# Performance work log

Measured on AMD Instinct MI355X. Metric: run time of the kernel, lower is better.

## Reference

```python
import jax, jax.numpy as jnp
import numpy as np

IN_CH, OUT_CH, K, UP = 512, 256, 3, 2
WSCALE = float(1.0 / np.sqrt(K * K * IN_CH))  # use_wscale gain / sqrt(fan_in), lr_mul=1
ACT_GAIN = float(np.sqrt(2.0))                # lrelu def_gain
CLAMP = 256.0                                  # conv_clamp * runtime_gain(=1)
FIR_PAD = 1                                    # px0+pxt = px1+pxt = 1 (derived in forward)

def _fir_filter():
    # upfirdn2d.setup_filter([1,3,3,1]): outer product then normalize to sum 1
    f1 = jnp.array([1.0, 3.0, 3.0, 1.0], jnp.float32)
    f2 = jnp.outer(f1, f1)
    return f2 / jnp.sum(f2)  # (4,4), sums to 1

def setup_inputs() -> dict:
    key = jax.random.key(0)
    k1, k2 = jax.random.split(key)
    return {
        "x": jax.random.normal(k1, (16, IN_CH, 64, 64), jnp.float32),
        "weight": jax.random.normal(k2, (OUT_CH, IN_CH, K, K), jnp.float32),
        "bias": jnp.zeros((OUT_CH,), jnp.float32),
    }

def _forward(x, weight, bias):
    w = weight * WSCALE  # runtime weight scaling
    # torch conv_transpose2d(x, w.transpose(0,1), stride=UP, padding=0)
    # == lhs-dilated correlation with spatially flipped kernel, pad K-1 each side
    k = w[:, :, ::-1, ::-1]
    y = jax.lax.conv_general_dilated(
        x, k, window_strides=(1, 1),
        padding=((K - 1, K - 1), (K - 1, K - 1)),
        lhs_dilation=(UP, UP),
        dimension_numbers=('NCHW', 'OIHW', 'NCHW'))  # (N, OUT_CH, 129, 129)
    # upfirdn2d(up=1, padding=(1,1,1,1), gain=UP**2):
    # pad, then depthwise conv with flipped filter scaled by gain**(ndim/2)=UP*UP
    f = _fir_filter() * (UP * UP)
    y = jnp.pad(y, ((0, 0), (0, 0), (FIR_PAD, FIR_PAD), (FIR_PAD, FIR_PAD)))
    fk = jnp.broadcast_to(f[::-1, ::-1][None, None], (OUT_CH, 1, 4, 4))
    y = jax.lax.conv_general_dilated(
        y, fk, (1, 1), 'VALID',
        feature_group_count=OUT_CH,
        dimension_numbers=('NCHW', 'OIHW', 'NCHW'))  # (N, OUT_CH, 128, 128)
    # bias_act: bias add, leaky_relu(0.2), gain sqrt(2), clamp +-256
    y = y + bias[None, :, None, None]
    y = jnp.where(y >= 0, y, 0.2 * y) * ACT_GAIN
    return jnp.clip(y, -CLAMP, CLAMP)

def reference(x, weight, bias):
    return _forward(x, weight, bias)
```

## Files before the change

### kernel.cpp

```cpp
#include <hip/hip_runtime.h>
#include <hip/hip_bf16.h>

#define NIMG 16
#define IN_CH 512
#define OUT_CH 256
#define HIN 64
#define HOUT 128
#define HP 66

#define WSCALE 0.014731391f
#define ACT_GAIN 1.41421356237f
#define CLAMP_V 256.0f

typedef __attribute__((ext_vector_type(8))) short bf16x8;
typedef __attribute__((ext_vector_type(4))) float f32x4;
typedef __attribute__((ext_vector_type(16))) float f32x16;

__device__ __constant__ float c_G[2][3][3] = {
    {{0.00f, 0.25f, 0.75f}, {0.75f, 0.75f, 0.25f}, {0.25f, 0.00f, 0.00f}},
    {{0.00f, 0.00f, 0.25f}, {0.25f, 0.75f, 0.75f}, {0.75f, 0.25f, 0.00f}}
};

#define XBF_BYTES ((size_t)NIMG * 64 * HP * HP * 16)
#define EBF_BYTES ((size_t)9 * 64 * 1024 * 16)
#define WS_NEED (XBF_BYTES + EBF_BYTES)

__global__ __launch_bounds__(256) void xpose_kernel(const float* __restrict__ x,
                                                    __hip_bfloat16* __restrict__ xbf) {
    const int n = blockIdx.z;
    const int hp = blockIdx.y;
    const int c0 = blockIdx.x << 6;
    const int tid = threadIdx.x;
    const int sgb = c0 >> 3;
    const bf16x8 zero = {0, 0, 0, 0, 0, 0, 0, 0};

    if (hp == 0 || hp == HP - 1) {
        for (int idx = tid; idx < 8 * HP; idx += 256) {
            int s3 = idx / HP, wp = idx - s3 * HP;
            size_t a = (((size_t)(n * 64 + sgb + s3) * HP + hp) * HP + wp);
            *(bf16x8*)((char*)xbf + a * 16) = zero;
        }
        return;
    }
    __shared__ float tile[64][65];
    {
        int cc = tid >> 6, w = tid & 63;
        for (int cb = 0; cb < 64; cb += 4)
            tile[cb + cc][w] =
                x[(((size_t)n * IN_CH + c0 + cb + cc) * HIN + (hp - 1)) * HIN + w];
    }
    __syncthreads();
    {
        int s3 = tid >> 5, wq = tid & 31;
#pragma unroll
        for (int wb = 0; wb < 64; wb += 32) {
            int wimg = wb + wq;
            bf16x8 v;
#pragma unroll
            for (int k = 0; k < 8; ++k) {
                __hip_bfloat16 b = __float2bfloat16(tile[s3 * 8 + k][wimg]);
                v[k] = *reinterpret_cast<short*>(&b);
            }
            size_t a = (((size_t)(n * 64 + sgb + s3) * HP + hp) * HP + (wimg + 1));
            *(bf16x8*)((char*)xbf + a * 16) = v;
        }
        if (tid < 16) {
            int s3h = tid >> 1, wph = (tid & 1) ? (HP - 1) : 0;
            size_t a = (((size_t)(n * 64 + sgb + s3h) * HP + hp) * HP + wph);
            *(bf16x8*)((char*)xbf + a * 16) = zero;
        }
    }
}

__global__ __launch_bounds__(256) void build_ebf_kernel(const float* __restrict__ w,
                                                        __hip_bfloat16* __restrict__ ebf) {
    int gid = blockIdx.x * 256 + threadIdx.x;
    if (gid >= OUT_CH * IN_CH) return;
    int oc = gid >> 9, c = gid & 511;
    int sg = c >> 3, ce = c & 7;
    float wm[3][3];
    const float* wp = w + (size_t)gid * 9;
#pragma unroll
    for (int a = 0; a < 3; ++a)
#pragma unroll
        for (int b = 0; b < 3; ++b) wm[a][b] = wp[a * 3 + b] * WSCALE;
#pragma unroll
    for (int i = 0; i < 3; ++i)
#pragma unroll
        for (int j = 0; j < 3; ++j)
#pragma unroll
            for (int pu = 0; pu < 2; ++pu)
#pragma unroll
                for (int pv = 0; pv < 2; ++pv) {
                    float s = 0.f;
#pragma unroll
                    for (int a = 0; a < 3; ++a)
#pragma unroll
                        for (int b = 0; b < 3; ++b)
                            s += wm[a][b] * c_G[pu][i][a] * c_G[pv][j][b];
                    int row = oc * 4 + pu * 2 + pv;
                    ebf[(((size_t)(i * 3 + j) * 64 + sg) * 1024 + row) * 8 + ce] =
                        __float2bfloat16(s);
                }
}

#define MFMA8(AF, BF, MH)                                                                   \
    do {                                                                                    \
        acc[(MH)*4+0] = __builtin_amdgcn_mfma_f32_32x32x16_bf16((AF)[0], (BF)[0], acc[(MH)*4+0], 0, 0, 0); \
        acc[(MH)*4+1] = __builtin_amdgcn_mfma_f32_32x32x16_bf16((AF)[0], (BF)[2], acc[(MH)*4+1], 0, 0, 0); \
        acc[(MH)*4+2] = __builtin_amdgcn_mfma_f32_32x32x16_bf16((AF)[2], (BF)[0], acc[(MH)*4+2], 0, 0, 0); \
        acc[(MH)*4+3] = __builtin_amdgcn_mfma_f32_32x32x16_bf16((AF)[2], (BF)[2], acc[(MH)*4+3], 0, 0, 0); \
        acc[(MH)*4+0] = __builtin_amdgcn_mfma_f32_32x32x16_bf16((AF)[1], (BF)[1], acc[(MH)*4+0], 0, 0, 0); \
        acc[(MH)*4+1] = __builtin_amdgcn_mfma_f32_32x32x16_bf16((AF)[1], (BF)[3], acc[(MH)*4+1], 0, 0, 0); \
        acc[(MH)*4+2] = __builtin_amdgcn_mfma_f32_32x32x16_bf16((AF)[3], (BF)[1], acc[(MH)*4+2], 0, 0, 0); \
        acc[(MH)*4+3] = __builtin_amdgcn_mfma_f32_32x32x16_bf16((AF)[3], (BF)[3], acc[(MH)*4+3], 0, 0, 0); \
    } while (0)

#define CDA 4224
#define CDB 1024
#define ASTEP 557568
#define AJ_FJ (-3902960)
#define AJ_FI (-3901952)
#define BSTEP 131072
#define DAK1(PAR) (((((PAR) ^ 1) << 2) | 1) << 14)
#define DBK1(PAR) (((((PAR) ^ 1) << 2) | 3) << 14)
#define DAK0(PAR) ((((PAR) << 2) | 0) << 14)
#define DBK0(PAR) ((((PAR) << 2) | 2) << 14)

#define GLL(SRC, DSTOFF)                                                          \
    __builtin_amdgcn_global_load_lds(                                             \
        (const __attribute__((address_space(1))) unsigned int*)(SRC),             \
        (__attribute__((address_space(3))) unsigned int*)(ldsW + (DSTOFF)), 16, 0, 0)

#define TILE_ITER(PAR, TT, SP01, SP23, VMS, LGK3, LAST)                           \
    {                                                                             \
        const int A0 = (PAR) ? aM0O : aM0E;                                       \
        const int A1 = (PAR) ? aM1O : aM1E;                                       \
        const int B0 = (PAR) ? bN0O : bN0E;                                       \
        const int B1 = (PAR) ? bN1O : bN1E;                                       \
        \
        afO[0] = *(const bf16x8*)&lds[A0 + 1024];                                 \
        afO[1] = *(const bf16x8*)&lds[A0 + 1024 + 8192];                          \
        afO[2] = *(const bf16x8*)&lds[A1 + 1024];                                 \
        afO[3] = *(const bf16x8*)&lds[A1 + 1024 + 8192];                          \
        if (SP01) { GLL(xbc + sA1 + voffA, DAK1(PAR));                            \
                    GLL(xbc + sA1 + voffA + CDA, DAK1(PAR) + 1024); }             \
        sA1 += (((TT) & 7) == 6) ? (((TT) == 22 || (TT) == 46) ? AJ_FI : AJ_FJ)   \
                                 : ASTEP;                                         \
        asm volatile("s_waitcnt lgkmcnt(4)" ::: "memory");                        \
        __builtin_amdgcn_sched_barrier(0);                                        \
        __builtin_amdgcn_s_setprio(1);                                            \
        MFMA8(afE, b0, 0);                                                        \
        __builtin_amdgcn_s_setprio(0);                                            \
        asm volatile("s_waitcnt " VMS ::: "memory");                              \
        __builtin_amdgcn_s_barrier();                                             \
        __builtin_amdgcn_sched_barrier(0);                                        \
          \
        afE[0] = *(const bf16x8*)&lds[A0 + 16384];                                \
        afE[1] = *(const bf16x8*)&lds[A0 + 16384 + 8192];                         \
        afE[2] = *(const bf16x8*)&lds[A1 + 16384];                                \
        afE[3] = *(const bf16x8*)&lds[A1 + 16384 + 8192];                         \
        b1[0] = *(const bf16x8*)&lds[B0 + 16384];                                 \
        b1[1] = *(const bf16x8*)&lds[B0 + 16384 + 8192];                          \
        b1[2] = *(const bf16x8*)&lds[B1 + 16384];                                 \
        b1[3] = *(const bf16x8*)&lds[B1 + 16384 + 8192];                          \
        if (SP01) { GLL(ebc + sB1 + voffB, DBK1(PAR));                            \
                    GLL(ebc + sB1 + voffB + CDB, DBK1(PAR) + 1024); }             \
        sB1 += BSTEP;                                                             \
        asm volatile("s_waitcnt lgkmcnt(8)" ::: "memory");                        \
        __builtin_amdgcn_sched_barrier(0);                                        \
        __builtin_amdgcn_s_setprio(1);                                            \
        MFMA8(afO, b0, 1);                                                        \
        __builtin_amdgcn_s_setprio(0);                                            \
        __builtin_amdgcn_s_barrier();                                             \
        __builtin_amdgcn_sched_barrier(0);                                        \
        \
        afO[0] = *(const bf16x8*)&lds[A0 + 16384 + 1024];                         \
        afO[1] = *(const bf16x8*)&lds[A0 + 16384 + 1024 + 8192];                  \
        afO[2] = *(const bf16x8*)&lds[A1 + 16384 + 1024];                         \
        afO[3] = *(const bf16x8*)&lds[A1 + 16384 + 1024 + 8192];                  \
        if (SP23) { GLL(xbc + sA0 + voffA, DAK0(PAR));                            \
                    GLL(xbc + sA0 + voffA + CDA, DAK0(PAR) + 1024); }             \
        sA0 += (((TT) & 7) == 5) ? (((TT) == 21 || (TT) == 45) ? AJ_FI : AJ_FJ)   \
                                 : ASTEP;                                         \
        asm volatile("s_waitcnt lgkmcnt(4)" ::: "memory");                        \
        __builtin_amdgcn_sched_barrier(0);                                        \
        __builtin_amdgcn_s_setprio(1);                                            \
        MFMA8(afE, b1, 0);                                                        \
        __builtin_amdgcn_s_setprio(0);                                            \
        asm volatile("s_waitcnt " VMS ::: "memory");                              \
        __builtin_amdgcn_s_barrier();                                             \
        __builtin_amdgcn_sched_barrier(0);                                        \
           \
        if (!(LAST)) {                                                            \
            const int nA0 = (PAR) ? aM0E : aM0O;                                  \
            const int nA1 = (PAR) ? aM1E : aM1O;                                  \
            const int nB0 = (PAR) ? bN0E : bN0O;                                  \
            const int nB1 = (PAR) ? bN1E : bN1O;                                  \
            afE[0] = *(const bf16x8*)&lds[nA0];                                   \
            afE[1] = *(const bf16x8*)&lds[nA0 + 8192];                            \
            afE[2] = *(const bf16x8*)&lds[nA1];                                   \
            afE[3] = *(const bf16x8*)&lds[nA1 + 8192];                            \
            b0[0] = *(const bf16x8*)&lds[nB0];                                    \
            b0[1] = *(const bf16x8*)&lds[nB0 + 8192];                             \
            b0[2] = *(const bf16x8*)&lds[nB1];                                    \
            b0[3] = *(const bf16x8*)&lds[nB1 + 8192];                             \
        }                                                                         \
        if (SP23) { GLL(ebc + sB0 + voffB, DBK0(PAR));                            \
                    GLL(ebc + sB0 + voffB + CDB, DBK0(PAR) + 1024); }             \
        sB0 += BSTEP;                                                             \
        asm volatile("s_waitcnt " LGK3 ::: "memory");                             \
        __builtin_amdgcn_sched_barrier(0);                                        \
        __builtin_amdgcn_s_setprio(1);                                            \
        MFMA8(afO, b1, 1);                                                        \
        __builtin_amdgcn_s_setprio(0);                                            \
        __builtin_amdgcn_s_barrier();                                             \
        __builtin_amdgcn_sched_barrier(0);                                        \
    }

__global__ __launch_bounds__(512, 2) void mfma_conv8_kernel(
    const __hip_bfloat16* __restrict__ xbf, const __hip_bfloat16* __restrict__ ebf,
    const float* __restrict__ bias, float* __restrict__ out) {
    __shared__ __align__(16) char lds[131072];

    const int tid = threadIdx.x;
    const int lane = tid & 63;
    const int wid = tid >> 6;
    const int wy = wid >> 2;
    const int wx = wid & 3;

    const int bid = blockIdx.x;
    const int wkid = ((bid & 7) << 7) + (bid >> 3);
    const int mtile = wkid >> 2;
    const int ntile = wkid & 3;
    const int n = mtile >> 4;
    const int sub = mtile & 15;
    const int qh0 = (sub >> 2) << 4;
    const int qw0 = (sub & 3) << 4;
    const int n0 = ntile << 8;

    const int slice = wid & 3;
    const int rowhalf = wid >> 2;

    f32x16 acc[8];
#pragma unroll
    for (int j = 0; j < 8; ++j) acc[j] = (f32x16)(0.f);

    char* ldsW = lds + (slice << 12) + (rowhalf << 11);
    const char* xbc = (const char*)xbf;
    const char* ebc = (const char*)ebf;

    const int q = lane ^ ((lane & 32) ? 4 : 0) ^ ((slice & 1) ? 4 : 0);
    const int voffA =
        ((((n << 6) + slice) * HP + qh0 + (rowhalf << 3) + (q >> 4)) * HP + qw0 +
         (q & 15)) * 16;
    const int voffB = (slice << 14) + ((n0 + (rowhalf << 7) + q) << 4);

    auto stage = [&](int s) {
        const int tt2 = s >> 2;
        const int part = s & 3;
        const int mat = part & 1;
        const int kh = part >> 1;
        const int slot = (((tt2 & 1) << 2) | (mat << 1) | kh) << 14;
        const int sgoff = (tt2 << 3) + (kh << 2);
#pragma unroll
        for (int c = 0; c < 2; ++c) {
            const char* src = mat == 0 ? (xbc + voffA + sgoff * 69696 + c * CDA)
                                       : (ebc + voffB + sgoff * 16384 + c * CDB);
            __builtin_amdgcn_global_load_lds(
                (const __attribute__((address_space(1))) unsigned int*)src,
                (__attribute__((address_space(3))) unsigned int*)(ldsW + slot + c * 1024),
                16, 0, 0);
        }
    };

    const int sl = lane >> 5;
    const int l31 = lane & 31;
    const int sx = sl ? 64 : 0;
    const int aM0E = (sl << 12) + (wy << 11) + ((l31 << 4) ^ sx);
    const int aM1E = (sl << 12) + (wy << 11) + 512 + ((l31 << 4) ^ 64 ^ sx);
    const int aM0O = aM0E + 65536;
    const int aM1O = aM1E + 65536;
    const int bN0E = 32768 + (sl << 12) + (wx << 10) + ((l31 << 4) ^ sx);
    const int bN1E = 32768 + (sl << 12) + (wx << 10) + 512 + ((l31 << 4) ^ 64 ^ sx);
    const int bN0O = bN0E + 65536;
    const int bN1O = bN1E + 65536;

    int sA1 = 12 * 69696;
    int sA0 = 16 * 69696;
    int sB1 = 12 * 16384;
    int sB0 = 16 * 16384;

#pragma unroll
    for (int s = 0; s < 6; ++s) stage(s);
    asm volatile("s_waitcnt vmcnt(8)" ::: "memory");
    __builtin_amdgcn_s_barrier();
    __builtin_amdgcn_sched_barrier(0);

    bf16x8 afE[4], afO[4], b0[4], b1[4];
    afE[0] = *(const bf16x8*)&lds[aM0E];
    afE[1] = *(const bf16x8*)&lds[aM0E + 8192];
    afE[2] = *(const bf16x8*)&lds[aM1E];
    afE[3] = *(const bf16x8*)&lds[aM1E + 8192];
    b0[0] = *(const bf16x8*)&lds[bN0E];
    b0[1] = *(const bf16x8*)&lds[bN0E + 8192];
    b0[2] = *(const bf16x8*)&lds[bN1E];
    b0[3] = *(const bf16x8*)&lds[bN1E + 8192];

#pragma unroll 1
    for (int tt = 0; tt < 68; tt += 2) {
        TILE_ITER(0, tt, 1, 1, "vmcnt(6)", "lgkmcnt(8)", 0);
        TILE_ITER(1, tt + 1, 1, 1, "vmcnt(6)", "lgkmcnt(8)", 0);
    }
    TILE_ITER(0, 68, 1, 1, "vmcnt(6)", "lgkmcnt(8)", 0);
    TILE_ITER(1, 69, 1, 1, "vmcnt(0)", "lgkmcnt(8)", 0);
    TILE_ITER(0, 70, 1, 0, "vmcnt(0)", "lgkmcnt(8)", 0);
    TILE_ITER(1, 71, 0, 0, "vmcnt(0)", "lgkmcnt(0)", 1);

    float bv[2];
#pragma unroll
    for (int nt = 0; nt < 2; ++nt)
        bv[nt] = bias[(n0 + (wx << 6) + (nt << 5) + l31) >> 2];
#pragma unroll
    for (int j = 0; j < 8; ++j) {
        const int mt = j >> 1, nt = j & 1;
        const int nn = n0 + (wx << 6) + (nt << 5) + l31;
        const int oc = nn >> 2, pu = (nn >> 1) & 1, pv = nn & 1;
#pragma unroll
        for (int v = 0; v < 16; ++v) {
            const int m = (wy << 7) + (mt << 5) + (v & 3) + ((v >> 2) << 3) + (sl << 2);
            const int qr = m >> 4, qc = m & 15;
            const int hb = 2 * (qh0 + qr), wb = 2 * (qw0 + qc);
            float val = acc[j][v] + bv[nt];
            val = (val >= 0.f ? val : 0.2f * val) * ACT_GAIN;
            val = fminf(fmaxf(val, -CLAMP_V), CLAMP_V);
            out[(((size_t)n * OUT_CH + oc) * HOUT + (hb + pu)) * HOUT + (wb + pv)] = val;
        }
    }
}

__global__ void build_e_kernel(const float* __restrict__ w, float* __restrict__ e_ws) {
    int gid = blockIdx.x * blockDim.x + threadIdx.x;
    if (gid >= OUT_CH * IN_CH) return;
    float wm[3][3];
    const float* wp = w + (size_t)gid * 9;
#pragma unroll
    for (int a = 0; a < 3; ++a)
#pragma unroll
        for (int b = 0; b < 3; ++b) wm[a][b] = wp[a * 3 + b] * WSCALE;
    float* op = e_ws + (size_t)gid * 36;
#pragma unroll
    for (int i = 0; i < 3; ++i)
#pragma unroll
        for (int j = 0; j < 3; ++j)
#pragma unroll
            for (int pu = 0; pu < 2; ++pu)
#pragma unroll
                for (int pv = 0; pv < 2; ++pv) {
                    float s = 0.f;
#pragma unroll
                    for (int a = 0; a < 3; ++a)
#pragma unroll
                        for (int b = 0; b < 3; ++b)
                            s += wm[a][b] * c_G[pu][i][a] * c_G[pv][j][b];
                    op[(i * 3 + j) * 4 + pu * 2 + pv] = s;
                }
}

#define OGB 8
#define CB 8
#define QT 16
__global__ __launch_bounds__(256) void fused_conv_kernel(
    const float* __restrict__ x, const float* __restrict__ e_ws,
    const float* __restrict__ bias, float* __restrict__ out) {
    __shared__ float sX[CB][18][19];
    __shared__ float4 sE[OGB * CB * 9];
    const int tid = threadIdx.x;
    const int o2 = tid >> 7;
    const int qy = (tid >> 3) & 15;
    const int qxp = tid & 7;
    const int tileIdx = blockIdx.x;
    const int hq0 = (tileIdx >> 2) * QT;
    const int wq0 = (tileIdx & 3) * QT;
    const int o0 = blockIdx.y * OGB;
    const int n = blockIdx.z;
    float4 acc[2][4];
#pragma unroll
    for (int q = 0; q < 2; ++q)
#pragma unroll
        for (int oo = 0; oo < 4; ++oo) acc[q][oo] = make_float4(0.f, 0.f, 0.f, 0.f);
    for (int c0 = 0; c0 < IN_CH; c0 += CB) {
        for (int idx = tid; idx < CB * 18 * 18; idx += 256) {
            int cc = idx / 324;
            int rem = idx - cc * 324;
            int r = rem / 18;
            int col = rem - r * 18;
            int h = hq0 - 1 + r;
            int ww = wq0 - 1 + col;
            float v = 0.f;
            if (h >= 0 && h < HIN && ww >= 0 && ww < HIN)
                v = x[(((size_t)n * IN_CH + (c0 + cc)) * HIN + h) * HIN + ww];
            sX[cc][r][col] = v;
        }
        {
            float* sEf = (float*)sE;
            for (int idx = tid; idx < OGB * CB * 36; idx += 256) {
                int ol = idx / (CB * 36);
                int rem = idx - ol * (CB * 36);
                sEf[ol * (CB * 36) + rem] =
                    e_ws[((size_t)(o0 + ol) * IN_CH + c0) * 36 + rem];
            }
        }
        __syncthreads();
#pragma unroll 1
        for (int cc = 0; cc < CB; ++cc) {
#pragma unroll
            for (int i = 0; i < 3; ++i) {
#pragma unroll
                for (int j = 0; j < 3; ++j) {
                    float xv0 = sX[cc][qy + i][2 * qxp + j];
                    float xv1 = sX[cc][qy + i][2 * qxp + 1 + j];
#pragma unroll
                    for (int oo = 0; oo < 4; ++oo) {
                        float4 e = sE[((o2 * 4 + oo) * CB + cc) * 9 + i * 3 + j];
                        acc[0][oo].x += xv0 * e.x; acc[0][oo].y += xv0 * e.y;
                        acc[0][oo].z += xv0 * e.z; acc[0][oo].w += xv0 * e.w;
                        acc[1][oo].x += xv1 * e.x; acc[1][oo].y += xv1 * e.y;
                        acc[1][oo].z += xv1 * e.z; acc[1][oo].w += xv1 * e.w;
                    }
                }
            }
        }
        __syncthreads();
    }
#pragma unroll
    for (int q = 0; q < 2; ++q) {
        int qx = 2 * qxp + q;
        int u0 = 2 * (hq0 + qy);
        int v0 = 2 * (wq0 + qx);
#pragma unroll
        for (int oo = 0; oo < 4; ++oo) {
            int o = o0 + o2 * 4 + oo;
            float b = bias[o];
            float vals[4] = {acc[q][oo].x, acc[q][oo].y, acc[q][oo].z, acc[q][oo].w};
#pragma unroll
            for (int p = 0; p < 4; ++p) {
                int pu = p >> 1, pv = p & 1;
                float v = vals[p] + b;
                v = (v >= 0.f ? v : 0.2f * v) * ACT_GAIN;
                v = fminf(fmaxf(v, -CLAMP_V), CLAMP_V);
                out[(((size_t)n * OUT_CH + o) * HOUT + (u0 + pu)) * HOUT + (v0 + pv)] = v;
            }
        }
    }
}

extern "C" void kernel_launch(void* const* d_in, const int* in_sizes, int n_in,
                              void* d_out, int out_size, void* d_ws, size_t ws_size,
                              hipStream_t stream) {
    const float* x = (const float*)d_in[0];
    const float* w = (const float*)d_in[1];
    const float* bias = (const float*)d_in[2];
    float* out = (float*)d_out;

    if (ws_size >= WS_NEED) {
        __hip_bfloat16* xbf = (__hip_bfloat16*)d_ws;
        __hip_bfloat16* ebf = (__hip_bfloat16*)((char*)d_ws + XBF_BYTES);
        xpose_kernel<<<dim3(8, HP, NIMG), 256, 0, stream>>>(x, xbf);
        build_ebf_kernel<<<(OUT_CH * IN_CH + 255) / 256, 256, 0, stream>>>(w, ebf);
        mfma_conv8_kernel<<<dim3(1024), 512, 0, stream>>>(xbf, ebf, bias, out);
    } else {
        float* e_ws = (float*)d_ws;
        build_e_kernel<<<(OUT_CH * IN_CH + 255) / 256, 256, 0, stream>>>(w, e_ws);
        dim3 grid(16, OUT_CH / OGB, NIMG);
        fused_conv_kernel<<<grid, 256, 0, stream>>>(x, e_ws, bias, out);
    }
}
```

Measured before the change: 629.6 us.

## Halve LDS footprint with single-buffered in-place refill pipeline

Replaces the double-buffered (even/odd parity) 128KB LDS staging with a single 64KB buffer. Each half-slot is refilled right after its fragments are read into registers, so prefetch depth drops to about one half-tile ahead. The smaller LDS allocation may allow more resident workgroups or waves per CU, while less prefetch distance risks exposing global-load latency at the vmcnt waits.

```diff
diff --git a/kernel.cpp b/kernel.cpp
--- a/kernel.cpp
+++ b/kernel.cpp
@@ -122,95 +122,83 @@
 #define AJ_FJ (-3902960)
 #define AJ_FI (-3901952)
 #define BSTEP 131072
-#define DAK1(PAR) (((((PAR) ^ 1) << 2) | 1) << 14)
-#define DBK1(PAR) (((((PAR) ^ 1) << 2) | 3) << 14)
-#define DAK0(PAR) ((((PAR) << 2) | 0) << 14)
-#define DBK0(PAR) ((((PAR) << 2) | 2) << 14)
 
 #define GLL(SRC, DSTOFF)                                                          \
     __builtin_amdgcn_global_load_lds(                                             \
         (const __attribute__((address_space(1))) unsigned int*)(SRC),             \
         (__attribute__((address_space(3))) unsigned int*)(ldsW + (DSTOFF)), 16, 0, 0)
 
-#define TILE_ITER(PAR, TT, SP01, SP23, VMS, LGK3, LAST)                           \
+#define TILE_ITER(TT, SP, VM0, VM2, LGK3, LAST)                                   \
     {                                                                             \
-        const int A0 = (PAR) ? aM0O : aM0E;                                       \
-        const int A1 = (PAR) ? aM1O : aM1E;                                       \
-        const int B0 = (PAR) ? bN0O : bN0E;                                       \
-        const int B1 = (PAR) ? bN1O : bN1E;                                       \
-        \
-        afO[0] = *(const bf16x8*)&lds[A0 + 1024];                                 \
-        afO[1] = *(const bf16x8*)&lds[A0 + 1024 + 8192];                          \
-        afO[2] = *(const bf16x8*)&lds[A1 + 1024];                                 \
-        afO[3] = *(const bf16x8*)&lds[A1 + 1024 + 8192];                          \
-        if (SP01) { GLL(xbc + sA1 + voffA, DAK1(PAR));                            \
-                    GLL(xbc + sA1 + voffA + CDA, DAK1(PAR) + 1024); }             \
-        sA1 += (((TT) & 7) == 6) ? (((TT) == 22 || (TT) == 46) ? AJ_FI : AJ_FJ)   \
-                                 : ASTEP;                                         \
+         \
+        afO[0] = *(const bf16x8*)&lds[aM0 + 1024];                                \
+        afO[1] = *(const bf16x8*)&lds[aM0 + 1024 + 8192];                         \
+        afO[2] = *(const bf16x8*)&lds[aM1 + 1024];                                \
+        afO[3] = *(const bf16x8*)&lds[aM1 + 1024 + 8192];                         \
         asm volatile("s_waitcnt lgkmcnt(4)" ::: "memory");                        \
         __builtin_amdgcn_sched_barrier(0);                                        \
+        if (SP) { GLL(ebc + sB0 + voffB, 32768);                                  \
+                  GLL(ebc + sB0 + voffB + CDB, 32768 + 1024); }                   \
+        sB0 += BSTEP;                                                             \
         __builtin_amdgcn_s_setprio(1);                                            \
         MFMA8(afE, b0, 0);                                                        \
         __builtin_amdgcn_s_setprio(0);                                            \
-        asm volatile("s_waitcnt " VMS ::: "memory");                              \
+        asm volatile("s_waitcnt " VM0 ::: "memory");                              \
         __builtin_amdgcn_s_barrier();                                             \
         __builtin_amdgcn_sched_barrier(0);                                        \
           \
-        afE[0] = *(const bf16x8*)&lds[A0 + 16384];                                \
-        afE[1] = *(const bf16x8*)&lds[A0 + 16384 + 8192];                         \
-        afE[2] = *(const bf16x8*)&lds[A1 + 16384];                                \
-        afE[3] = *(const bf16x8*)&lds[A1 + 16384 + 8192];                         \
-        b1[0] = *(const bf16x8*)&lds[B0 + 16384];                                 \
-        b1[1] = *(const bf16x8*)&lds[B0 + 16384 + 8192];                          \
-        b1[2] = *(const bf16x8*)&lds[B1 + 16384];                                 \
-        b1[3] = *(const bf16x8*)&lds[B1 + 16384 + 8192];                          \
-        if (SP01) { GLL(ebc + sB1 + voffB, DBK1(PAR));                            \
-                    GLL(ebc + sB1 + voffB + CDB, DBK1(PAR) + 1024); }             \
-        sB1 += BSTEP;                                                             \
+        afE[0] = *(const bf16x8*)&lds[aM0 + 16384];                               \
+        afE[1] = *(const bf16x8*)&lds[aM0 + 16384 + 8192];                        \
+        afE[2] = *(const bf16x8*)&lds[aM1 + 16384];                               \
+        afE[3] = *(const bf16x8*)&lds[aM1 + 16384 + 8192];                        \
+        b1[0] = *(const bf16x8*)&lds[bN0 + 16384];                                \
+        b1[1] = *(const bf16x8*)&lds[bN0 + 16384 + 8192];                         \
+        b1[2] = *(const bf16x8*)&lds[bN1 + 16384];                                \
+        b1[3] = *(const bf16x8*)&lds[bN1 + 16384 + 8192];                         \
         asm volatile("s_waitcnt lgkmcnt(8)" ::: "memory");                        \
         __builtin_amdgcn_sched_barrier(0);                                        \
+        if (SP) { GLL(xbc + sA0 + voffA, 0);                                      \
+                  GLL(xbc + sA0 + voffA + CDA, 1024); }                           \
+        sA0 += (((TT) & 7) == 6) ? (((TT) == 22 || (TT) == 46) ? AJ_FI : AJ_FJ)   \
+                                 : ASTEP;                                         \
         __builtin_amdgcn_s_setprio(1);                                            \
         MFMA8(afO, b0, 1);                                                        \
         __builtin_amdgcn_s_setprio(0);                                            \
         __builtin_amdgcn_s_barrier();                                             \
         __builtin_amdgcn_sched_barrier(0);                                        \
-        \
-        afO[0] = *(const bf16x8*)&lds[A0 + 16384 + 1024];                         \
-        afO[1] = *(const bf16x8*)&lds[A0 + 16384 + 1024 + 8192];                  \
-        afO[2] = *(const bf16x8*)&lds[A1 + 16384 + 1024];                         \
-        afO[3] = *(const bf16x8*)&lds[A1 + 16384 + 1024 + 8192];                  \
-        if (SP23) { GLL(xbc + sA0 + voffA, DAK0(PAR));                            \
-                    GLL(xbc + sA0 + voffA + CDA, DAK0(PAR) + 1024); }             \
-        sA0 += (((TT) & 7) == 5) ? (((TT) == 21 || (TT) == 45) ? AJ_FI : AJ_FJ)   \
-                                 : ASTEP;                                         \
+         \
+        afO[0] = *(const bf16x8*)&lds[aM0 + 16384 + 1024];                        \
+        afO[1] = *(const bf16x8*)&lds[aM0 + 16384 + 1024 + 8192];                 \
+        afO[2] = *(const bf16x8*)&lds[aM1 + 16384 + 1024];                        \
+        afO[3] = *(const bf16x8*)&lds[aM1 + 16384 + 1024 + 8192];                 \
         asm volatile("s_waitcnt lgkmcnt(4)" ::: "memory");                        \
         __builtin_amdgcn_sched_barrier(0);                                        \
+        if (SP) { GLL(ebc + sB1 + voffB, 49152);                                  \
+                  GLL(ebc + sB1 + voffB + CDB, 49152 + 1024); }                   \
+        sB1 += BSTEP;                                                             \
         __builtin_amdgcn_s_setprio(1);                                            \
         MFMA8(afE, b1, 0);                                                        \
         __builtin_amdgcn_s_setprio(0);                                            \
-        asm volatile("s_waitcnt " VMS ::: "memory");                              \
+        asm volatile("s_waitcnt " VM2 ::: "memory");                              \
         __builtin_amdgcn_s_barrier();                                             \
         __builtin_amdgcn_sched_barrier(0);                                        \
            \
         if (!(LAST)) {                                                            \
-            const int nA0 = (PAR) ? aM0E : aM0O;                                  \
-            const int nA1 = (PAR) ? aM1E : aM1O;                                  \
-            const int nB0 = (PAR) ? bN0E : bN0O;                                  \
-            const int nB1 = (PAR) ? bN1E : bN1O;                                  \
-            afE[0] = *(const bf16x8*)&lds[nA0];                                   \
-            afE[1] = *(const bf16x8*)&lds[nA0 + 8192];                            \
-            afE[2] = *(const bf16x8*)&lds[nA1];                                   \
-            afE[3] = *(const bf16x8*)&lds[nA1 + 8192];                            \
-            b0[0] = *(const bf16x8*)&lds[nB0];                                    \
-            b0[1] = *(const bf16x8*)&lds[nB0 + 8192];                             \
-            b0[2] = *(const bf16x8*)&lds[nB1];                                    \
-            b0[3] = *(const bf16x8*)&lds[nB1 + 8192];                             \
+            afE[0] = *(const bf16x8*)&lds[aM0];                                   \
+            afE[1] = *(const bf16x8*)&lds[aM0 + 8192];                            \
+            afE[2] = *(const bf16x8*)&lds[aM1];                                   \
+            afE[3] = *(const bf16x8*)&lds[aM1 + 8192];                            \
+            b0[0] = *(const bf16x8*)&lds[bN0];                                    \
+            b0[1] = *(const bf16x8*)&lds[bN0 + 8192];                             \
+            b0[2] = *(const bf16x8*)&lds[bN1];                                    \
+            b0[3] = *(const bf16x8*)&lds[bN1 + 8192];                             \
         }                                                                         \
-        if (SP23) { GLL(ebc + sB0 + voffB, DBK0(PAR));                            \
-                    GLL(ebc + sB0 + voffB + CDB, DBK0(PAR) + 1024); }             \
-        sB0 += BSTEP;                                                             \
         asm volatile("s_waitcnt " LGK3 ::: "memory");                             \
         __builtin_amdgcn_sched_barrier(0);                                        \
+        if (SP) { GLL(xbc + sA1 + voffA, 16384);                                  \
+                  GLL(xbc + sA1 + voffA + CDA, 16384 + 1024); }                   \
+        sA1 += (((TT) & 7) == 6) ? (((TT) == 22 || (TT) == 46) ? AJ_FI : AJ_FJ)   \
+                                 : ASTEP;                                         \
         __builtin_amdgcn_s_setprio(1);                                            \
         MFMA8(afO, b1, 1);                                                        \
         __builtin_amdgcn_s_setprio(0);                                            \
@@ -221,7 +209,7 @@
 __global__ __launch_bounds__(512, 2) void mfma_conv8_kernel(
     const __hip_bfloat16* __restrict__ xbf, const __hip_bfloat16* __restrict__ ebf,
     const float* __restrict__ bias, float* __restrict__ out) {
-    __shared__ __align__(16) char lds[131072];
+    __shared__ __align__(16) char lds[65536];
 
     const int tid = threadIdx.x;
     const int lane = tid & 63;
@@ -256,66 +244,46 @@
          (q & 15)) * 16;
     const int voffB = (slice << 14) + ((n0 + (rowhalf << 7) + q) << 4);
 
-    auto stage = [&](int s) {
-        const int tt2 = s >> 2;
-        const int part = s & 3;
-        const int mat = part & 1;
-        const int kh = part >> 1;
-        const int slot = (((tt2 & 1) << 2) | (mat << 1) | kh) << 14;
-        const int sgoff = (tt2 << 3) + (kh << 2);
-#pragma unroll
-        for (int c = 0; c < 2; ++c) {
-            const char* src = mat == 0 ? (xbc + voffA + sgoff * 69696 + c * CDA)
-                                       : (ebc + voffB + sgoff * 16384 + c * CDB);
-            __builtin_amdgcn_global_load_lds(
-                (const __attribute__((address_space(1))) unsigned int*)src,
-                (__attribute__((address_space(3))) unsigned int*)(ldsW + slot + c * 1024),
-                16, 0, 0);
-        }
-    };
-
     const int sl = lane >> 5;
     const int l31 = lane & 31;
     const int sx = sl ? 64 : 0;
-    const int aM0E = (sl << 12) + (wy << 11) + ((l31 << 4) ^ sx);
-    const int aM1E = (sl << 12) + (wy << 11) + 512 + ((l31 << 4) ^ 64 ^ sx);
-    const int aM0O = aM0E + 65536;
-    const int aM1O = aM1E + 65536;
-    const int bN0E = 32768 + (sl << 12) + (wx << 10) + ((l31 << 4) ^ sx);
-    const int bN1E = 32768 + (sl << 12) + (wx << 10) + 512 + ((l31 << 4) ^ 64 ^ sx);
-    const int bN0O = bN0E + 65536;
-    const int bN1O = bN1E + 65536;
-
+    const int aM0 = (sl << 12) + (wy << 11) + ((l31 << 4) ^ sx);
+    const int aM1 = (sl << 12) + (wy << 11) + 512 + ((l31 << 4) ^ 64 ^ sx);
+    const int bN0 = 32768 + (sl << 12) + (wx << 10) + ((l31 << 4) ^ sx);
+    const int bN1 = 32768 + (sl << 12) + (wx << 10) + 512 + ((l31 << 4) ^ 64 ^ sx);
+
+    int sA0 = 8 * 69696;
     int sA1 = 12 * 69696;
-    int sA0 = 16 * 69696;
+    int sB0 = 8 * 16384;
     int sB1 = 12 * 16384;
-    int sB0 = 16 * 16384;
-
-#pragma unroll
-    for (int s = 0; s < 6; ++s) stage(s);
-    asm volatile("s_waitcnt vmcnt(8)" ::: "memory");
+
+    GLL(xbc + voffA, 0);
+    GLL(xbc + voffA + CDA, 1024);
+    GLL(ebc + voffB, 32768);
+    GLL(ebc + voffB + CDB, 32768 + 1024);
+    GLL(xbc + voffA + 4 * 69696, 16384);
+    GLL(xbc + voffA + 4 * 69696 + CDA, 16384 + 1024);
+    GLL(ebc + voffB + 4 * 16384, 49152);
+    GLL(ebc + voffB + 4 * 16384 + CDB, 49152 + 1024);
+    asm volatile("s_waitcnt vmcnt(4)" ::: "memory");
     __builtin_amdgcn_s_barrier();
     __builtin_amdgcn_sched_barrier(0);
 
     bf16x8 afE[4], afO[4], b0[4], b1[4];
-    afE[0] = *(const bf16x8*)&lds[aM0E];
-    afE[1] = *(const bf16x8*)&lds[aM0E + 8192];
-    afE[2] = *(const bf16x8*)&lds[aM1E];
-    afE[3] = *(const bf16x8*)&lds[aM1E + 8192];
-    b0[0] = *(const bf16x8*)&lds[bN0E];
-    b0[1] = *(const bf16x8*)&lds[bN0E + 8192];
-    b0[2] = *(const bf16x8*)&lds[bN1E];
-    b0[3] = *(const bf16x8*)&lds[bN1E + 8192];
+    afE[0] = *(const bf16x8*)&lds[aM0];
+    afE[1] = *(const bf16x8*)&lds[aM0 + 8192];
+    afE[2] = *(const bf16x8*)&lds[aM1];
+    afE[3] = *(const bf16x8*)&lds[aM1 + 8192];
+    b0[0] = *(const bf16x8*)&lds[bN0];
+    b0[1] = *(const bf16x8*)&lds[bN0 + 8192];
+    b0[2] = *(const bf16x8*)&lds[bN1];
+    b0[3] = *(const bf16x8*)&lds[bN1 + 8192];
 
 #pragma unroll 1
-    for (int tt = 0; tt < 68; tt += 2) {
-        TILE_ITER(0, tt, 1, 1, "vmcnt(6)", "lgkmcnt(8)", 0);
-        TILE_ITER(1, tt + 1, 1, 1, "vmcnt(6)", "lgkmcnt(8)", 0);
-    }
-    TILE_ITER(0, 68, 1, 1, "vmcnt(6)", "lgkmcnt(8)", 0);
-    TILE_ITER(1, 69, 1, 1, "vmcnt(0)", "lgkmcnt(8)", 0);
-    TILE_ITER(0, 70, 1, 0, "vmcnt(0)", "lgkmcnt(8)", 0);
-    TILE_ITER(1, 71, 0, 0, "vmcnt(0)", "lgkmcnt(0)", 1);
+    for (int tt = 0; tt < 71; ++tt) {
+        TILE_ITER(tt, 1, "vmcnt(2)", "vmcnt(2)", "lgkmcnt(8)", 0);
+    }
+    TILE_ITER(71, 0, "vmcnt(0)", "vmcnt(0)", "lgkmcnt(0)", 1);
 
     float bv[2];
 #pragma unroll
```

After: 650.2 us. 3.3% more time.

## Split conv8 block across 16 waves with smaller per-wave MFMA tiles

Applied to the files above, without the earlier changes.

The MFMA conv kernel goes from 512 to 1024 threads per block. Each wave's accumulator tile is halved (4 instead of 8 32x32 accumulators), and the K-step fragment loads are restructured to match. Each wave now issues one global_load_lds per stage instead of two, and the LDS offsets, waitcnt thresholds and epilogue row mapping are updated accordingly. The aim is more waves to hide latency and lower register pressure per wave. In exchange there are more barriers per unit of work, more LDS fragment reads per MFMA, and launch_bounds loses the two-blocks-per-CU hint.

```diff
diff --git a/kernel.cpp b/kernel.cpp
--- a/kernel.cpp
+++ b/kernel.cpp
@@ -104,20 +104,14 @@
                 }
 }
 
-#define MFMA8(AF, BF, MH)                                                                   \
+#define MFMA4(AF, BF)                                                                       \
     do {                                                                                    \
-        acc[(MH)*4+0] = __builtin_amdgcn_mfma_f32_32x32x16_bf16((AF)[0], (BF)[0], acc[(MH)*4+0], 0, 0, 0); \
-        acc[(MH)*4+1] = __builtin_amdgcn_mfma_f32_32x32x16_bf16((AF)[0], (BF)[2], acc[(MH)*4+1], 0, 0, 0); \
-        acc[(MH)*4+2] = __builtin_amdgcn_mfma_f32_32x32x16_bf16((AF)[2], (BF)[0], acc[(MH)*4+2], 0, 0, 0); \
-        acc[(MH)*4+3] = __builtin_amdgcn_mfma_f32_32x32x16_bf16((AF)[2], (BF)[2], acc[(MH)*4+3], 0, 0, 0); \
-        acc[(MH)*4+0] = __builtin_amdgcn_mfma_f32_32x32x16_bf16((AF)[1], (BF)[1], acc[(MH)*4+0], 0, 0, 0); \
-        acc[(MH)*4+1] = __builtin_amdgcn_mfma_f32_32x32x16_bf16((AF)[1], (BF)[3], acc[(MH)*4+1], 0, 0, 0); \
-        acc[(MH)*4+2] = __builtin_amdgcn_mfma_f32_32x32x16_bf16((AF)[3], (BF)[1], acc[(MH)*4+2], 0, 0, 0); \
-        acc[(MH)*4+3] = __builtin_amdgcn_mfma_f32_32x32x16_bf16((AF)[3], (BF)[3], acc[(MH)*4+3], 0, 0, 0); \
+        acc[0] = __builtin_amdgcn_mfma_f32_32x32x16_bf16((AF)[0], (BF)[0], acc[0], 0, 0, 0);\
+        acc[1] = __builtin_amdgcn_mfma_f32_32x32x16_bf16((AF)[0], (BF)[1], acc[1], 0, 0, 0);\
+        acc[2] = __builtin_amdgcn_mfma_f32_32x32x16_bf16((AF)[1], (BF)[0], acc[2], 0, 0, 0);\
+        acc[3] = __builtin_amdgcn_mfma_f32_32x32x16_bf16((AF)[1], (BF)[1], acc[3], 0, 0, 0);\
     } while (0)
 
-#define CDA 4224
-#define CDB 1024
 #define ASTEP 557568
 #define AJ_FJ (-3902960)
 #define AJ_FI (-3901952)
@@ -134,91 +128,73 @@
 
 #define TILE_ITER(PAR, TT, SP01, SP23, VMS, LGK3, LAST)                           \
     {                                                                             \
-        const int A0 = (PAR) ? aM0O : aM0E;                                       \
-        const int A1 = (PAR) ? aM1O : aM1E;                                       \
-        const int B0 = (PAR) ? bN0O : bN0E;                                       \
-        const int B1 = (PAR) ? bN1O : bN1E;                                       \
-        \
-        afO[0] = *(const bf16x8*)&lds[A0 + 1024];                                 \
-        afO[1] = *(const bf16x8*)&lds[A0 + 1024 + 8192];                          \
-        afO[2] = *(const bf16x8*)&lds[A1 + 1024];                                 \
-        afO[3] = *(const bf16x8*)&lds[A1 + 1024 + 8192];                          \
-        if (SP01) { GLL(xbc + sA1 + voffA, DAK1(PAR));                            \
-                    GLL(xbc + sA1 + voffA + CDA, DAK1(PAR) + 1024); }             \
+        const int PB = (PAR) ? 65536 : 0;                                         \
+                     \
+        aO[0] = *(const bf16x8*)&lds[A0 + PB + 8192];                             \
+        aO[1] = *(const bf16x8*)&lds[A1 + PB + 8192];                             \
+        bO[0] = *(const bf16x8*)&lds[B0 + PB + 8192];                             \
+        bO[1] = *(const bf16x8*)&lds[B1 + PB + 8192];                             \
+        if (SP01) GLL(xbc + sA1 + voffA, DAK1(PAR));                              \
         sA1 += (((TT) & 7) == 6) ? (((TT) == 22 || (TT) == 46) ? AJ_FI : AJ_FJ)   \
                                  : ASTEP;                                         \
         asm volatile("s_waitcnt lgkmcnt(4)" ::: "memory");                        \
         __builtin_amdgcn_sched_barrier(0);                                        \
         __builtin_amdgcn_s_setprio(1);                                            \
-        MFMA8(afE, b0, 0);                                                        \
+        MFMA4(aE, bE);                                                            \
         __builtin_amdgcn_s_setprio(0);                                            \
         asm volatile("s_waitcnt " VMS ::: "memory");                              \
         __builtin_amdgcn_s_barrier();                                             \
         __builtin_amdgcn_sched_barrier(0);                                        \
-          \
-        afE[0] = *(const bf16x8*)&lds[A0 + 16384];                                \
-        afE[1] = *(const bf16x8*)&lds[A0 + 16384 + 8192];                         \
-        afE[2] = *(const bf16x8*)&lds[A1 + 16384];                                \
-        afE[3] = *(const bf16x8*)&lds[A1 + 16384 + 8192];                         \
-        b1[0] = *(const bf16x8*)&lds[B0 + 16384];                                 \
-        b1[1] = *(const bf16x8*)&lds[B0 + 16384 + 8192];                          \
-        b1[2] = *(const bf16x8*)&lds[B1 + 16384];                                 \
-        b1[3] = *(const bf16x8*)&lds[B1 + 16384 + 8192];                          \
-        if (SP01) { GLL(ebc + sB1 + voffB, DBK1(PAR));                            \
-                    GLL(ebc + sB1 + voffB + CDB, DBK1(PAR) + 1024); }             \
+                     \
+        aE[0] = *(const bf16x8*)&lds[A0 + PB + 16384];                            \
+        aE[1] = *(const bf16x8*)&lds[A1 + PB + 16384];                            \
+        bE[0] = *(const bf16x8*)&lds[B0 + PB + 16384];                            \
+        bE[1] = *(const bf16x8*)&lds[B1 + PB + 16384];                            \
+        if (SP01) GLL(ebc + sB1 + voffB, DBK1(PAR));                              \
         sB1 += BSTEP;                                                             \
-        asm volatile("s_waitcnt lgkmcnt(8)" ::: "memory");                        \
+        asm volatile("s_waitcnt lgkmcnt(4)" ::: "memory");                        \
         __builtin_amdgcn_sched_barrier(0);                                        \
         __builtin_amdgcn_s_setprio(1);                                            \
-        MFMA8(afO, b0, 1);                                                        \
+        MFMA4(aO, bO);                                                            \
         __builtin_amdgcn_s_setprio(0);                                            \
         __builtin_amdgcn_s_barrier();                                             \
         __builtin_amdgcn_sched_barrier(0);                                        \
-        \
-        afO[0] = *(const bf16x8*)&lds[A0 + 16384 + 1024];                         \
-        afO[1] = *(const bf16x8*)&lds[A0 + 16384 + 1024 + 8192];                  \
-        afO[2] = *(const bf16x8*)&lds[A1 + 16384 + 1024];                         \
-        afO[3] = *(const bf16x8*)&lds[A1 + 16384 + 1024 + 8192];                  \
-        if (SP23) { GLL(xbc + sA0 + voffA, DAK0(PAR));                            \
-                    GLL(xbc + sA0 + voffA + CDA, DAK0(PAR) + 1024); }             \
+                     \
+        aO[0] = *(const bf16x8*)&lds[A0 + PB + 24576];                            \
+        aO[1] = *(const bf16x8*)&lds[A1 + PB + 24576];                            \
+        bO[0] = *(const bf16x8*)&lds[B0 + PB + 24576];                            \
+        bO[1] = *(const bf16x8*)&lds[B1 + PB + 24576];                            \
+        if (SP23) GLL(xbc + sA0 + voffA, DAK0(PAR));                              \
         sA0 += (((TT) & 7) == 5) ? (((TT) == 21 || (TT) == 45) ? AJ_FI : AJ_FJ)   \
                                  : ASTEP;                                         \
         asm volatile("s_waitcnt lgkmcnt(4)" ::: "memory");                        \
         __builtin_amdgcn_sched_barrier(0);                                        \
         __builtin_amdgcn_s_setprio(1);                                            \
-        MFMA8(afE, b1, 0);                                                        \
+        MFMA4(aE, bE);                                                            \
         __builtin_amdgcn_s_setprio(0);                                            \
         asm volatile("s_waitcnt " VMS ::: "memory");                              \
         __builtin_amdgcn_s_barrier();                                             \
         __builtin_amdgcn_sched_barrier(0);                                        \
            \
         if (!(LAST)) {                                                            \
-            const int nA0 = (PAR) ? aM0E : aM0O;                                  \
-            const int nA1 = (PAR) ? aM1E : aM1O;                                  \
-            const int nB0 = (PAR) ? bN0E : bN0O;                                  \
-            const int nB1 = (PAR) ? bN1E : bN1O;                                  \
-            afE[0] = *(const bf16x8*)&lds[nA0];                                   \
-            afE[1] = *(const bf16x8*)&lds[nA0 + 8192];                            \
-            afE[2] = *(const bf16x8*)&lds[nA1];                                   \
-            afE[3] = *(const bf16x8*)&lds[nA1 + 8192];                            \
-            b0[0] = *(const bf16x8*)&lds[nB0];                                    \
-            b0[1] = *(const bf16x8*)&lds[nB0 + 8192];                             \
-            b0[2] = *(const bf16x8*)&lds[nB1];                                    \
-            b0[3] = *(const bf16x8*)&lds[nB1 + 8192];                             \
+            const int NB = (PAR) ? 0 : 65536;                                     \
+            aE[0] = *(const bf16x8*)&lds[A0 + NB];                                \
+            aE[1] = *(const bf16x8*)&lds[A1 + NB];                                \
+            bE[0] = *(const bf16x8*)&lds[B0 + NB];                                \
+            bE[1] = *(const bf16x8*)&lds[B1 + NB];                                \
         }                                                                         \
-        if (SP23) { GLL(ebc + sB0 + voffB, DBK0(PAR));                            \
-                    GLL(ebc + sB0 + voffB + CDB, DBK0(PAR) + 1024); }             \
+        if (SP23) GLL(ebc + sB0 + voffB, DBK0(PAR));                              \
         sB0 += BSTEP;                                                             \
         asm volatile("s_waitcnt " LGK3 ::: "memory");                             \
         __builtin_amdgcn_sched_barrier(0);                                        \
         __builtin_amdgcn_s_setprio(1);                                            \
-        MFMA8(afO, b1, 1);                                                        \
+        MFMA4(aO, bO);                                                            \
         __builtin_amdgcn_s_setprio(0);                                            \
         __builtin_amdgcn_s_barrier();                                             \
         __builtin_amdgcn_sched_barrier(0);                                        \
     }
 
-__global__ __launch_bounds__(512, 2) void mfma_conv8_kernel(
+__global__ __launch_bounds__(1024) void mfma_conv8_kernel(
     const __hip_bfloat16* __restrict__ xbf, const __hip_bfloat16* __restrict__ ebf,
     const float* __restrict__ bias, float* __restrict__ out) {
     __shared__ __align__(16) char lds[131072];
@@ -240,21 +216,21 @@
     const int n0 = ntile << 8;
 
     const int slice = wid & 3;
-    const int rowhalf = wid >> 2;
-
-    f32x16 acc[8];
-#pragma unroll
-    for (int j = 0; j < 8; ++j) acc[j] = (f32x16)(0.f);
-
-    char* ldsW = lds + (slice << 12) + (rowhalf << 11);
+    const int rb = wid >> 2;
+
+    f32x16 acc[4];
+#pragma unroll
+    for (int j = 0; j < 4; ++j) acc[j] = (f32x16)(0.f);
+
+    char* ldsW = lds + (slice << 12) + (rb << 10);
     const char* xbc = (const char*)xbf;
     const char* ebc = (const char*)ebf;
 
     const int q = lane ^ ((lane & 32) ? 4 : 0) ^ ((slice & 1) ? 4 : 0);
     const int voffA =
-        ((((n << 6) + slice) * HP + qh0 + (rowhalf << 3) + (q >> 4)) * HP + qw0 +
+        ((((n << 6) + slice) * HP + qh0 + (rb << 2) + (q >> 4)) * HP + qw0 +
          (q & 15)) * 16;
-    const int voffB = (slice << 14) + ((n0 + (rowhalf << 7) + q) << 4);
+    const int voffB = (slice << 14) + ((n0 + (rb << 6) + q) << 4);
 
     auto stage = [&](int s) {
         const int tt2 = s >> 2;
@@ -262,29 +238,19 @@
         const int mat = part & 1;
         const int kh = part >> 1;
         const int slot = (((tt2 & 1) << 2) | (mat << 1) | kh) << 14;
-        const int sgoff = (tt2 << 3) + (kh << 2);
-#pragma unroll
-        for (int c = 0; c < 2; ++c) {
-            const char* src = mat == 0 ? (xbc + voffA + sgoff * 69696 + c * CDA)
-                                       : (ebc + voffB + sgoff * 16384 + c * CDB);
-            __builtin_amdgcn_global_load_lds(
-                (const __attribute__((address_space(1))) unsigned int*)src,
-                (__attribute__((address_space(3))) unsigned int*)(ldsW + slot + c * 1024),
-                16, 0, 0);
-        }
+        const int sg = (tt2 << 3) + (kh << 2);
+        const char* src = mat == 0 ? (xbc + voffA + sg * 69696)
+                                   : (ebc + voffB + sg * 16384);
+        GLL(src, slot);
     };
 
     const int sl = lane >> 5;
     const int l31 = lane & 31;
     const int sx = sl ? 64 : 0;
-    const int aM0E = (sl << 12) + (wy << 11) + ((l31 << 4) ^ sx);
-    const int aM1E = (sl << 12) + (wy << 11) + 512 + ((l31 << 4) ^ 64 ^ sx);
-    const int aM0O = aM0E + 65536;
-    const int aM1O = aM1E + 65536;
-    const int bN0E = 32768 + (sl << 12) + (wx << 10) + ((l31 << 4) ^ sx);
-    const int bN1E = 32768 + (sl << 12) + (wx << 10) + 512 + ((l31 << 4) ^ 64 ^ sx);
-    const int bN0O = bN0E + 65536;
-    const int bN1O = bN1E + 65536;
+    const int A0 = (sl << 12) + (wy << 10) + ((l31 << 4) ^ sx);
+    const int A1 = (sl << 12) + (wy << 10) + 512 + ((l31 << 4) ^ 64 ^ sx);
+    const int B0 = 32768 + (sl << 12) + (wx << 10) + ((l31 << 4) ^ sx);
+    const int B1 = 32768 + (sl << 12) + (wx << 10) + 512 + ((l31 << 4) ^ 64 ^ sx);
 
     int sA1 = 12 * 69696;
     int sA0 = 16 * 69696;
@@ -293,28 +259,24 @@
 
 #pragma unroll
     for (int s = 0; s < 6; ++s) stage(s);
-    asm volatile("s_waitcnt vmcnt(8)" ::: "memory");
+    asm volatile("s_waitcnt vmcnt(2)" ::: "memory");
     __builtin_amdgcn_s_barrier();
     __builtin_amdgcn_sched_barrier(0);
 
-    bf16x8 afE[4], afO[4], b0[4], b1[4];
-    afE[0] = *(const bf16x8*)&lds[aM0E];
-    afE[1] = *(const bf16x8*)&lds[aM0E + 8192];
-    afE[2] = *(const bf16x8*)&lds[aM1E];
-    afE[3] = *(const bf16x8*)&lds[aM1E + 8192];
-    b0[0] = *(const bf16x8*)&lds[bN0E];
-    b0[1] = *(const bf16x8*)&lds[bN0E + 8192];
-    b0[2] = *(const bf16x8*)&lds[bN1E];
-    b0[3] = *(const bf16x8*)&lds[bN1E + 8192];
+    bf16x8 aE[2], aO[2], bE[2], bO[2];
+    aE[0] = *(const bf16x8*)&lds[A0];
+    aE[1] = *(const bf16x8*)&lds[A1];
+    bE[0] = *(const bf16x8*)&lds[B0];
+    bE[1] = *(const bf16x8*)&lds[B1];
 
 #pragma unroll 1
     for (int tt = 0; tt < 68; tt += 2) {
-        TILE_ITER(0, tt, 1, 1, "vmcnt(6)", "lgkmcnt(8)", 0);
-        TILE_ITER(1, tt + 1, 1, 1, "vmcnt(6)", "lgkmcnt(8)", 0);
-    }
-    TILE_ITER(0, 68, 1, 1, "vmcnt(6)", "lgkmcnt(8)", 0);
-    TILE_ITER(1, 69, 1, 1, "vmcnt(0)", "lgkmcnt(8)", 0);
-    TILE_ITER(0, 70, 1, 0, "vmcnt(0)", "lgkmcnt(8)", 0);
+        TILE_ITER(0, tt, 1, 1, "vmcnt(3)", "lgkmcnt(4)", 0);
+        TILE_ITER(1, tt + 1, 1, 1, "vmcnt(3)", "lgkmcnt(4)", 0);
+    }
+    TILE_ITER(0, 68, 1, 1, "vmcnt(3)", "lgkmcnt(4)", 0);
+    TILE_ITER(1, 69, 1, 1, "vmcnt(0)", "lgkmcnt(4)", 0);
+    TILE_ITER(0, 70, 1, 0, "vmcnt(0)", "lgkmcnt(4)", 0);
     TILE_ITER(1, 71, 0, 0, "vmcnt(0)", "lgkmcnt(0)", 1);
 
     float bv[2];
@@ -322,13 +284,13 @@
     for (int nt = 0; nt < 2; ++nt)
         bv[nt] = bias[(n0 + (wx << 6) + (nt << 5) + l31) >> 2];
 #pragma unroll
-    for (int j = 0; j < 8; ++j) {
+    for (int j = 0; j < 4; ++j) {
         const int mt = j >> 1, nt = j & 1;
         const int nn = n0 + (wx << 6) + (nt << 5) + l31;
         const int oc = nn >> 2, pu = (nn >> 1) & 1, pv = nn & 1;
 #pragma unroll
         for (int v = 0; v < 16; ++v) {
-            const int m = (wy << 7) + (mt << 5) + (v & 3) + ((v >> 2) << 3) + (sl << 2);
+            const int m = (wy << 6) + (mt << 5) + (v & 3) + ((v >> 2) << 3) + (sl << 2);
             const int qr = m >> 4, qc = m & 15;
             const int hb = 2 * (qh0 + qr), wb = 2 * (qw0 + qc);
             float val = acc[j][v] + bv[nt];
@@ -468,7 +430,7 @@
         __hip_bfloat16* ebf = (__hip_bfloat16*)((char*)d_ws + XBF_BYTES);
         xpose_kernel<<<dim3(8, HP, NIMG), 256, 0, stream>>>(x, xbf);
         build_ebf_kernel<<<(OUT_CH * IN_CH + 255) / 256, 256, 0, stream>>>(w, ebf);
-        mfma_conv8_kernel<<<dim3(1024), 512, 0, stream>>>(xbf, ebf, bias, out);
+        mfma_conv8_kernel<<<dim3(1024), 1024, 0, stream>>>(xbf, ebf, bias, out);
     } else {
         float* e_ws = (float*)d_ws;
         build_e_kernel<<<(OUT_CH * IN_CH + 255) / 256, 256, 0, stream>>>(w, e_ws);
```

Measured after the change: 651.3 us. +3.5%, slower.
